# Optimization experiments

Hardware: AMD Instinct MI355X
Metric: run time of the kernel (lower is better)

Reference implementation:

```python
import jax, jax.numpy as jnp
import numpy as np

IN_F, OUT_F = 4096, 4096
WBITS, GS, OFI = 3, 128, 128          # bitwidth, group_size, outfeature_interval
NG, NB = IN_F // GS, OUT_F // OFI     # 32 groups x 32 out-blocks
WPB = WBITS * GS * OFI // 32          # int32 words per (group, out-block) = 1536


def setup_inputs() -> dict:
    key = jax.random.key(0)
    k = jax.random.split(key, 6)
    x = jax.random.normal(k[0], (1, 128, IN_F), jnp.float32)
    qweight = jax.random.randint(k[1], (NG * NB * WPB,), 0, 2**31 - 1, jnp.int32)
    alpha = 0.02 * jax.random.uniform(k[2], (NG, OUT_F), jnp.float32) + 0.001
    beta = 0.001 * jax.random.normal(k[3], (NG, OUT_F), jnp.float32)
    block_bitwidth = jnp.full((NG, NB), WBITS, dtype=jnp.int32)   # uniform bitwidth
    offset = jnp.arange(NG * NB, dtype=jnp.int32) * WPB           # word start per block
    in_reorder = jax.random.permutation(k[4], IN_F).astype(jnp.int32)
    out_reorder = jax.random.permutation(k[5], OUT_F).astype(jnp.int32)
    return dict(x=x, qweight=qweight, alpha=alpha, beta=beta,
                block_bitwidth=block_bitwidth, offset=offset,
                in_reorder=in_reorder, out_reorder=out_reorder)


def _dequant(qweight, alpha, beta, offset):
    # gather each block's packed words via its offset
    idx = offset[:, None] + jnp.arange(WPB, dtype=jnp.int32)      # (NG*NB, WPB)
    words = qweight[idx].reshape(NG, NB, WBITS, GS * OFI // 32)
    # unpack 32 bits per word -> +-1 binary codes per bit-plane
    bits = (words[..., None] >> jnp.arange(32, dtype=jnp.int32)) & 1
    codes = bits.reshape(NG, NB, WBITS, GS, OFI).astype(jnp.float32) * 2.0 - 1.0
    plane = (2.0 ** jnp.arange(WBITS)).astype(jnp.float32)        # bit-plane weights
    q = jnp.einsum('gnbio,b->gnio', codes, plane)                 # (NG,NB,GS,OFI)
    a = alpha.reshape(NG, NB, OFI)[:, :, None, :]
    bt = beta.reshape(NG, NB, OFI)[:, :, None, :]
    w = q * a + bt                                                # per-group scale/shift
    return w.transpose(0, 2, 1, 3).reshape(IN_F, OUT_F)


def reference(x, qweight, alpha, beta, block_bitwidth, offset, in_reorder, out_reorder):
    # block_bitwidth is uniform (== WBITS) in this reference; dequant closes over WBITS
    w = _dequant(qweight, alpha, beta, offset)                    # (IN_F, OUT_F)
    B, T, _ = x.shape
    xf = x.reshape(-1, IN_F)[:, in_reorder]                       # input permutation
    y = (xf @ w)[:, out_reorder]                                  # matmul + out permutation
    return y.reshape(B, T, OUT_F)
```

## Files before the change

### kernel.cpp

```cpp
#include <hip/hip_runtime.h>
#include <hip/hip_bf16.h>
#include <stdint.h>

#define IN_F   4096
#define OUT_F  4096
#define NGRP   32
#define NBLK   32
#define GSZ    128
#define OFI    128
#define WPB    1536
#define M_TOK  128
#define KSPLIT 8
#define NTILE  64

typedef __attribute__((ext_vector_type(8))) short bf16x8;
typedef __attribute__((ext_vector_type(4))) float f32x4;

static __device__ __forceinline__ unsigned cvt_pk_bf16(float lo, float hi) {
    unsigned r;
    asm("v_cvt_pk_bf16_f32 %0, %1, %2" : "=v"(r) : "v"(lo), "v"(hi));
    return r;
}

__global__ __launch_bounds__(256) void k_prep(const float* __restrict__ x,
                                              const int* __restrict__ in_reorder,
                                              const int* __restrict__ out_reorder,
                                              const float* __restrict__ alpha,
                                              const float* __restrict__ beta,
                                              unsigned short* __restrict__ xr,
                                              int* __restrict__ inv_out,
                                              float* __restrict__ A2,
                                              float* __restrict__ B7) {
    int b = blockIdx.x;
    if (b < 512) {
        int idx = b * 256 + threadIdx.x;
        int t  = idx >> 10;
        int i0 = (idx & 1023) << 2;
        int4 src = *(const int4*)&in_reorder[i0];
        const float* row = x + (size_t)t * IN_F;
        float v0 = row[src.x], v1 = row[src.y], v2 = row[src.z], v3 = row[src.w];
        uint2 pk;
        pk.x = cvt_pk_bf16(v0, v1);
        pk.y = cvt_pk_bf16(v2, v3);
        *(uint2*)&xr[(size_t)t * IN_F + i0] = pk;
    } else if (b < 516) {
        int i0 = ((b - 512) * 256 + threadIdx.x) << 2;
        int4 o = *(const int4*)&out_reorder[i0];
        inv_out[o.x] = i0;
        inv_out[o.y] = i0 + 1;
        inv_out[o.z] = i0 + 2;
        inv_out[o.w] = i0 + 3;
    } else {
        int idx = ((b - 516) * 256 + threadIdx.x) << 2;
        float4 a = *(const float4*)&alpha[idx];
        float4 bt = *(const float4*)&beta[idx];
        float4 a2 = make_float4(2.f * a.x, 2.f * a.y, 2.f * a.z, 2.f * a.w);
        float4 b7 = make_float4(bt.x - 7.f * a.x, bt.y - 7.f * a.y,
                                bt.z - 7.f * a.z, bt.w - 7.f * a.w);
        *(float4*)&A2[idx] = a2;
        *(float4*)&B7[idx] = b7;
    }
}

__global__ __launch_bounds__(256, 2) void k_fused(const unsigned short* __restrict__ xr,
                                                  const int* __restrict__ qweight,
                                                  const float* __restrict__ A2,
                                                  const float* __restrict__ B7,
                                                  const int* __restrict__ offset,
                                                  float* __restrict__ Cpart) {
    __shared__ unsigned short Alds[128 * 128];
    __shared__ unsigned short Blds[NTILE * 128];
    const int nb  = blockIdx.x;
    const int ks  = blockIdx.y;
    const int n   = nb >> 1;
    const int wcb = (nb & 1) * 2;
    const int n0  = nb * NTILE;
    const int tid = threadIdx.x;
    const int l   = tid & 63;
    const int wid = tid >> 6;
    const int wm  = wid >> 1;
    const int wn  = wid & 1;

    const int p  = tid >> 2;
    const int wc = (tid >> 1) & 1;
    const int h  = tid & 1;
    const int wq = wcb + wc;
    const int io0 = 2 * p;

    f32x4 acc[4][2] = {};

    int cw0a, cw0b, cw1a, cw1b, cw2a, cw2b;
    {
        const int gb0 = (ks * 4) * NBLK + n;
        const int* q = qweight + offset[gb0];
        cw0a = q[ io0      * 4 + wq];
        cw0b = q[(io0 + 1) * 4 + wq];
        cw1a = q[ io0      * 4 + wq + 512];
        cw1b = q[(io0 + 1) * 4 + wq + 512];
        cw2a = q[ io0      * 4 + wq + 1024];
        cw2b = q[(io0 + 1) * 4 + wq + 1024];
    }

    #pragma unroll
    for (int kt = 0; kt < 4; ++kt) {
        const int g  = ks * 4 + kt;
        const int k0 = g * GSZ;

        #pragma unroll
        for (int c = 0; c < 8; ++c) {
            int e   = (c * 256 + tid) * 8;
            int row = e >> 7;
            int cb  = (e >> 3) & 15;
            uint4 v = *(const uint4*)&xr[(size_t)row * IN_F + k0 + (cb << 3)];
            *(uint4*)&Alds[row * 128 + ((cb ^ (row & 15)) << 3)] = v;
        }

        {
            const float* a2 = A2 + g * OUT_F + n0 + wc * 32 + h * 16;
            const float* b7 = B7 + g * OUT_F + n0 + wc * 32 + h * 16;
            unsigned* B32 = (unsigned*)Blds;
            #pragma unroll
            for (int j = 0; j < 16; ++j) {
                int jb  = h * 16 + j;
                int col = wc * 32 + jb;
                float sa = a2[j];
                float sb = b7[j];
                int na = ((cw0a >> jb) & 1) | (((cw1a >> jb) & 1) << 1) | (((cw2a >> jb) & 1) << 2);
                int nbq = ((cw0b >> jb) & 1) | (((cw1b >> jb) & 1) << 1) | (((cw2b >> jb) & 1) << 2);
                float va = (float)na  * sa + sb;
                float vb = (float)nbq * sa + sb;
                B32[col * 64 + (((p >> 2) ^ (col & 15)) << 2) + (p & 3)] = cvt_pk_bf16(va, vb);
            }
        }

        if (kt < 3) {
            const int gb1 = (ks * 4 + kt + 1) * NBLK + n;
            const int* q = qweight + offset[gb1];
            cw0a = q[ io0      * 4 + wq];
            cw0b = q[(io0 + 1) * 4 + wq];
            cw1a = q[ io0      * 4 + wq + 512];
            cw1b = q[(io0 + 1) * 4 + wq + 512];
            cw2a = q[ io0      * 4 + wq + 1024];
            cw2b = q[(io0 + 1) * 4 + wq + 1024];
        }
        __syncthreads();

        #pragma unroll
        for (int kk = 0; kk < 4; ++kk) {
            const int cb = kk * 4 + (l >> 4);
            bf16x8 af[4], bfr[2];
            #pragma unroll
            for (int m = 0; m < 4; ++m) {
                int row = wm * 64 + m * 16 + (l & 15);
                af[m] = *(const bf16x8*)&Alds[row * 128 + ((cb ^ (row & 15)) << 3)];
            }
            #pragma unroll
            for (int nn = 0; nn < 2; ++nn) {
                int cl = wn * 32 + nn * 16 + (l & 15);
                bfr[nn] = *(const bf16x8*)&Blds[cl * 128 + ((cb ^ (cl & 15)) << 3)];
            }
            #pragma unroll
            for (int m = 0; m < 4; ++m)
                #pragma unroll
                for (int nn = 0; nn < 2; ++nn)
                    acc[m][nn] = __builtin_amdgcn_mfma_f32_16x16x32_bf16(
                        af[m], bfr[nn], acc[m][nn], 0, 0, 0);
        }
        __syncthreads();
    }

    float* Cb = Cpart + (size_t)ks * (M_TOK * OUT_F);
    #pragma unroll
    for (int m = 0; m < 4; ++m) {
        int row = wm * 64 + m * 16 + ((l >> 4) << 2);
        #pragma unroll
        for (int nn = 0; nn < 2; ++nn) {
            int col = n0 + wn * 32 + nn * 16 + (l & 15);
            #pragma unroll
            for (int r = 0; r < 4; ++r)
                Cb[(size_t)(row + r) * OUT_F + col] = acc[m][nn][r];
        }
    }
}

__global__ __launch_bounds__(256) void k_reduce(const float* __restrict__ Cpart,
                                                const int* __restrict__ inv_out,
                                                float* __restrict__ out) {
    int idx = blockIdx.x * 256 + threadIdx.x;
    int t  = idx >> 10;
    int c0 = (idx & 1023) << 2;
    float4 s = make_float4(0.f, 0.f, 0.f, 0.f);
    #pragma unroll
    for (int ks = 0; ks < KSPLIT; ++ks) {
        float4 v = *(const float4*)&Cpart[(size_t)ks * (M_TOK * OUT_F) + (size_t)t * OUT_F + c0];
        s.x += v.x; s.y += v.y; s.z += v.z; s.w += v.w;
    }
    const int* op = &inv_out[c0];
    float* row = out + (size_t)t * OUT_F;
    row[op[0]] = s.x;
    row[op[1]] = s.y;
    row[op[2]] = s.z;
    row[op[3]] = s.w;
}

extern "C" void kernel_launch(void* const* d_in, const int* in_sizes, int n_in,
                              void* d_out, int out_size, void* d_ws, size_t ws_size,
                              hipStream_t stream) {
    const float* x           = (const float*)d_in[0];
    const int*   qweight     = (const int*)d_in[1];
    const float* alpha       = (const float*)d_in[2];
    const float* beta        = (const float*)d_in[3];
    const int*   offset      = (const int*)d_in[5];
    const int*   in_reorder  = (const int*)d_in[6];
    const int*   out_reorder = (const int*)d_in[7];
    float* out = (float*)d_out;

    char* ws = (char*)d_ws;
    unsigned short* xr      = (unsigned short*)ws;
    float*          Cpart   = (float*)(ws + (1u << 20));
    int*            inv_out = (int*)(ws + (1u << 20) + (16u << 20));
    float*          A2      = (float*)(ws + (1u << 20) + (16u << 20) + (16u << 10));
    float*          B7      = A2 + NGRP * OUT_F;

    k_prep<<<dim3(644), dim3(256), 0, stream>>>(x, in_reorder, out_reorder,
                                                alpha, beta, xr, inv_out, A2, B7);
    k_fused<<<dim3(64, KSPLIT), dim3(256), 0, stream>>>(xr, qweight, A2, B7, offset, Cpart);
    k_reduce<<<dim3(512), dim3(256), 0, stream>>>(Cpart, inv_out, out);
}
```

Measured before the change: 31.56 us.

## Load activation tiles directly into LDS and widen prep gather

The activation tile copy in the fused GEMM now uses global_load_lds (direct global-to-LDS DMA), with the XOR swizzle applied on the source address so the LDS layout is unchanged. This removes the VGPR round trip and the ds_write instructions. The barrier moves to before the next-group qweight prefetch, and the MFMA loop runs at raised wave priority via s_setprio. The prep kernel also gathers eight inputs per thread with 16-byte stores, halving its grid. The main risk is correctness of the lane-to-LDS mapping that global_load_lds imposes.

```diff
diff --git a/kernel.cpp b/kernel.cpp
--- a/kernel.cpp
+++ b/kernel.cpp
@@ -22,6 +22,12 @@
     return r;
 }
 
+static __device__ __forceinline__ void gload_lds16(const void* g, void* s) {
+    __builtin_amdgcn_global_load_lds(
+        (const __attribute__((address_space(1))) unsigned int*)g,
+        (__attribute__((address_space(3))) unsigned int*)s, 16, 0, 0);
+}
+
 __global__ __launch_bounds__(256) void k_prep(const float* __restrict__ x,
                                               const int* __restrict__ in_reorder,
                                               const int* __restrict__ out_reorder,
@@ -32,26 +38,30 @@
                                               float* __restrict__ A2,
                                               float* __restrict__ B7) {
     int b = blockIdx.x;
-    if (b < 512) {
+    if (b < 256) {
         int idx = b * 256 + threadIdx.x;
-        int t  = idx >> 10;
-        int i0 = (idx & 1023) << 2;
-        int4 src = *(const int4*)&in_reorder[i0];
+        int t  = idx >> 9;
+        int i0 = (idx & 511) << 3;
+        int4 s0 = *(const int4*)&in_reorder[i0];
+        int4 s1 = *(const int4*)&in_reorder[i0 + 4];
         const float* row = x + (size_t)t * IN_F;
-        float v0 = row[src.x], v1 = row[src.y], v2 = row[src.z], v3 = row[src.w];
-        uint2 pk;
+        float v0 = row[s0.x], v1 = row[s0.y], v2 = row[s0.z], v3 = row[s0.w];
+        float v4 = row[s1.x], v5 = row[s1.y], v6 = row[s1.z], v7 = row[s1.w];
+        uint4 pk;
         pk.x = cvt_pk_bf16(v0, v1);
         pk.y = cvt_pk_bf16(v2, v3);
-        *(uint2*)&xr[(size_t)t * IN_F + i0] = pk;
-    } else if (b < 516) {
-        int i0 = ((b - 512) * 256 + threadIdx.x) << 2;
+        pk.z = cvt_pk_bf16(v4, v5);
+        pk.w = cvt_pk_bf16(v6, v7);
+        *(uint4*)&xr[(size_t)t * IN_F + i0] = pk;
+    } else if (b < 260) {
+        int i0 = ((b - 256) * 256 + threadIdx.x) << 2;
         int4 o = *(const int4*)&out_reorder[i0];
         inv_out[o.x] = i0;
         inv_out[o.y] = i0 + 1;
         inv_out[o.z] = i0 + 2;
         inv_out[o.w] = i0 + 3;
     } else {
-        int idx = ((b - 516) * 256 + threadIdx.x) << 2;
+        int idx = ((b - 260) * 256 + threadIdx.x) << 2;
         float4 a = *(const float4*)&alpha[idx];
         float4 bt = *(const float4*)&beta[idx];
         float4 a2 = make_float4(2.f * a.x, 2.f * a.y, 2.f * a.z, 2.f * a.w);
@@ -87,6 +97,9 @@
     const int wq = wcb + wc;
     const int io0 = 2 * p;
 
+    const int rl = l >> 4;
+    const int cl = l & 15;
+
     f32x4 acc[4][2] = {};
 
     int cw0a, cw0b, cw1a, cw1b, cw2a, cw2b;
@@ -107,12 +120,10 @@
         const int k0 = g * GSZ;
 
         #pragma unroll
-        for (int c = 0; c < 8; ++c) {
-            int e   = (c * 256 + tid) * 8;
-            int row = e >> 7;
-            int cb  = (e >> 3) & 15;
-            uint4 v = *(const uint4*)&xr[(size_t)row * IN_F + k0 + (cb << 3)];
-            *(uint4*)&Alds[row * 128 + ((cb ^ (row & 15)) << 3)] = v;
+        for (int i = 0; i < 8; ++i) {
+            int R = wid * 32 + i * 4 + rl;
+            const unsigned short* src = xr + ((size_t)R << 12) + k0 + ((cl ^ (R & 15)) << 3);
+            gload_lds16(src, (char*)Alds + wid * 8192 + i * 1024);
         }
 
         {
@@ -125,13 +136,14 @@
                 int col = wc * 32 + jb;
                 float sa = a2[j];
                 float sb = b7[j];
-                int na = ((cw0a >> jb) & 1) | (((cw1a >> jb) & 1) << 1) | (((cw2a >> jb) & 1) << 2);
+                int na  = ((cw0a >> jb) & 1) | (((cw1a >> jb) & 1) << 1) | (((cw2a >> jb) & 1) << 2);
                 int nbq = ((cw0b >> jb) & 1) | (((cw1b >> jb) & 1) << 1) | (((cw2b >> jb) & 1) << 2);
                 float va = (float)na  * sa + sb;
                 float vb = (float)nbq * sa + sb;
                 B32[col * 64 + (((p >> 2) ^ (col & 15)) << 2) + (p & 3)] = cvt_pk_bf16(va, vb);
             }
         }
+        __syncthreads();
 
         if (kt < 3) {
             const int gb1 = (ks * 4 + kt + 1) * NBLK + n;
@@ -143,8 +155,8 @@
             cw2a = q[ io0      * 4 + wq + 1024];
             cw2b = q[(io0 + 1) * 4 + wq + 1024];
         }
-        __syncthreads();
-
+
+        __builtin_amdgcn_s_setprio(1);
         #pragma unroll
         for (int kk = 0; kk < 4; ++kk) {
             const int cb = kk * 4 + (l >> 4);
@@ -156,8 +168,8 @@
             }
             #pragma unroll
             for (int nn = 0; nn < 2; ++nn) {
-                int cl = wn * 32 + nn * 16 + (l & 15);
-                bfr[nn] = *(const bf16x8*)&Blds[cl * 128 + ((cb ^ (cl & 15)) << 3)];
+                int clr = wn * 32 + nn * 16 + (l & 15);
+                bfr[nn] = *(const bf16x8*)&Blds[clr * 128 + ((cb ^ (clr & 15)) << 3)];
             }
             #pragma unroll
             for (int m = 0; m < 4; ++m)
@@ -166,6 +178,7 @@
                     acc[m][nn] = __builtin_amdgcn_mfma_f32_16x16x32_bf16(
                         af[m], bfr[nn], acc[m][nn], 0, 0, 0);
         }
+        __builtin_amdgcn_s_setprio(0);
         __syncthreads();
     }
 
@@ -222,7 +235,7 @@
     float*          A2      = (float*)(ws + (1u << 20) + (16u << 20) + (16u << 10));
     float*          B7      = A2 + NGRP * OUT_F;
 
-    k_prep<<<dim3(644), dim3(256), 0, stream>>>(x, in_reorder, out_reorder,
+    k_prep<<<dim3(388), dim3(256), 0, stream>>>(x, in_reorder, out_reorder,
                                                 alpha, beta, xr, inv_out, A2, B7);
     k_fused<<<dim3(64, KSPLIT), dim3(256), 0, stream>>>(xr, qweight, A2, B7, offset, Cpart);
     k_reduce<<<dim3(512), dim3(256), 0, stream>>>(Cpart, inv_out, out);
```

Measured after the change: 33.17 us. +5.1%, slower.
